# Optimization experiments

Measured on AMD Instinct MI355X. Metric: run time of the kernel, lower is better.

The kernel has to match this reference:

```python
import jax, jax.numpy as jnp
import numpy as np

B, LC, LS, D = 16384, 100, 12, 10  # C:(B,LC,D), x1:(B,LS,D)


def setup_inputs() -> dict:
    key = jax.random.key(0)
    ks = jax.random.split(key, 7)
    u = lambda k, shp: jax.random.uniform(k, shp, jnp.float32, -0.05, 0.05)  # keras 'uniform' init
    return {
        "C": jax.random.normal(ks[0], (B, LC, D), jnp.float32),
        "x1": jax.random.normal(ks[1], (B, LS, D), jnp.float32),
        "W": u(ks[2], (D, D)),      # kernelW (10,10)
        "Ws": u(ks[3], (LS, LS)),   # kernelWs (12,12)
        "Wc": u(ks[4], (LC, LC)),   # kernelWc (100,100)
        "Was": u(ks[5], (D, 1)),    # kernelas (10,1)
        "Wac": u(ks[6], (D, 1)),    # kernelac (10,1)
    }


def reference(C, x1, W, Ws, Wc, Was, Wac):
    # C: (B,100,10), x1: (B,12,10)
    RNN = jnp.swapaxes(x1, 1, 2)                      # (B,10,12)
    f = jnp.einsum('bld,de->ble', C, W)               # (B,100,10)
    F = jnp.tanh(jnp.matmul(f, RNN))                  # (B,100,12)
    s = jnp.einsum('bdl,lm->bdm', RNN, Ws)            # (B,10,12)
    c = jnp.einsum('bdl,lm->bdm', jnp.swapaxes(C, 1, 2), Wc)  # (B,10,100)
    Hs = jnp.tanh(s + jnp.matmul(c, F))               # (B,10,12)
    Hc = jnp.tanh(c + jnp.matmul(s, jnp.swapaxes(F, 1, 2)))   # (B,10,100)
    # softmax over the last (size-1) axis, exactly as K.softmax does here
    As = jax.nn.softmax(jnp.einsum('bdl,do->blo', Hs, Was), axis=-1)  # (B,12,1)
    Ac = jax.nn.softmax(jnp.einsum('bdl,do->blo', Hc, Wac), axis=-1)  # (B,100,1)
    As = jnp.swapaxes(As, 1, 2)                       # (B,1,12)
    Ac = jnp.swapaxes(Ac, 1, 2)                       # (B,1,100)
    sfinal = jnp.matmul(As, jnp.swapaxes(RNN, 1, 2))  # (B,1,10)
    cfinal = jnp.matmul(Ac, C)                        # (B,1,10)
    return jnp.concatenate([sfinal, cfinal], axis=-1) # (B,1,20)
```

## Files before the change

### kernel.cpp

```cpp
#include <hip/hip_runtime.h>
#include <hip/hip_bf16.h>


#define BATCHES 16384

__global__ __launch_bounds__(256) void coattention_sum_kernel(
    const float* __restrict__ C,
    const float* __restrict__ x1,
    float* __restrict__ out)
{
    const int t = threadIdx.x;
    const int lane = t & 63;
    const int q = lane >> 4;
    const int wave = t >> 6;
    const int u = blockIdx.x * 64 + wave * 16 + (lane & 15);
    const int b = u / 5;
    const int p = u - b * 5;

    const float2* __restrict__ cp =
        reinterpret_cast<const float2*>(C) + (size_t)b * 500 + q * 125 + p;
    const float2* __restrict__ xp =
        reinterpret_cast<const float2*>(x1) + (size_t)b * 60 + q * 15 + p;

    float sx = 0.f, sy = 0.f;
#pragma unroll
    for (int l = 0; l < 3; ++l)  { float2 v = xp[l * 5]; sx += v.x; sy += v.y; }

    float cx = 0.f, cy = 0.f;
#pragma unroll
    for (int l = 0; l < 25; ++l) { float2 v = cp[l * 5]; cx += v.x; cy += v.y; }

    sx += __shfl_xor(sx, 16); sy += __shfl_xor(sy, 16);
    cx += __shfl_xor(cx, 16); cy += __shfl_xor(cy, 16);
    sx += __shfl_xor(sx, 32); sy += __shfl_xor(sy, 32);
    cx += __shfl_xor(cx, 32); cy += __shfl_xor(cy, 32);

    if (q == 0) {
        float2* o = reinterpret_cast<float2*>(out) + (size_t)b * 10;
        o[p]     = make_float2(sx, sy);
        o[5 + p] = make_float2(cx, cy);
    }
}

extern "C" void kernel_launch(void* const* d_in, const int* in_sizes, int n_in,
                              void* d_out, int out_size, void* d_ws, size_t ws_size,
                              hipStream_t stream) {
    const float* C  = (const float*)d_in[0];
    const float* x1 = (const float*)d_in[1];
    float* out = (float*)d_out;

    const int units = BATCHES * 5;
    const int grid = units / 64;
    coattention_sum_kernel<<<grid, 256, 0, stream>>>(C, x1, out);
}
```

Before: 17.91 us.

## Stage batch tiles through LDS with coalesced float4 loads before reducing

```diff
diff --git a/kernel.cpp b/kernel.cpp
--- a/kernel.cpp
+++ b/kernel.cpp
@@ -3,40 +3,54 @@
 
 
 #define BATCHES 16384
+#define NB 16
 
-__global__ __launch_bounds__(256) void coattention_sum_kernel(
-    const float* __restrict__ C,
-    const float* __restrict__ x1,
+__global__ __launch_bounds__(320) void coattention_sum_kernel(
+    const float4* __restrict__ C4,
+    const float4* __restrict__ x14,
     float* __restrict__ out)
 {
+    __shared__ __align__(16) float4 lds4[NB * 250 + NB * 30];
+
     const int t = threadIdx.x;
-    const int lane = t & 63;
-    const int q = lane >> 4;
-    const int wave = t >> 6;
-    const int u = blockIdx.x * 64 + wave * 16 + (lane & 15);
-    const int b = u / 5;
-    const int p = u - b * 5;
 
-    const float2* __restrict__ cp =
-        reinterpret_cast<const float2*>(C) + (size_t)b * 500 + q * 125 + p;
-    const float2* __restrict__ xp =
-        reinterpret_cast<const float2*>(x1) + (size_t)b * 60 + q * 15 + p;
+    const float4* __restrict__ Cg = C4 + (size_t)blockIdx.x * (NB * 250);
+    const float4* __restrict__ Xg = x14 + (size_t)blockIdx.x * (NB * 30);
+#pragma unroll
+    for (int k = 0; k < 12; ++k)
+        lds4[k * 320 + t] = Cg[k * 320 + t];
+    if (t < 160)
+        lds4[3840 + t] = Cg[3840 + t];
+    lds4[4000 + t] = Xg[t];
+    if (t < 160)
+        lds4[4320 + t] = Xg[320 + t];
+    __syncthreads();
+
+    const int unit = t >> 2;
+    const int q = t & 3;
+    const int b = unit / 5;
+    const int p = unit - b * 5;
+
+    const float2* __restrict__ lbase = reinterpret_cast<const float2*>(lds4);
+    const float2* __restrict__ lc = lbase + b * 500 + q * 125 + p;
+    const float2* __restrict__ lx = lbase + 8000 + b * 60 + q * 15 + p;
+
+    float cx = 0.f, cy = 0.f;
+#pragma unroll
+    for (int l = 0; l < 25; ++l) { float2 v = lc[l * 5]; cx += v.x; cy += v.y; }
 
     float sx = 0.f, sy = 0.f;
 #pragma unroll
-    for (int l = 0; l < 3; ++l)  { float2 v = xp[l * 5]; sx += v.x; sy += v.y; }
+    for (int l = 0; l < 3; ++l)  { float2 v = lx[l * 5]; sx += v.x; sy += v.y; }
 
-    float cx = 0.f, cy = 0.f;
-#pragma unroll
-    for (int l = 0; l < 25; ++l) { float2 v = cp[l * 5]; cx += v.x; cy += v.y; }
-
-    sx += __shfl_xor(sx, 16); sy += __shfl_xor(sy, 16);
-    cx += __shfl_xor(cx, 16); cy += __shfl_xor(cy, 16);
-    sx += __shfl_xor(sx, 32); sy += __shfl_xor(sy, 32);
-    cx += __shfl_xor(cx, 32); cy += __shfl_xor(cy, 32);
+    cx += __shfl_xor(cx, 1); cy += __shfl_xor(cy, 1);
+    sx += __shfl_xor(sx, 1); sy += __shfl_xor(sy, 1);
+    cx += __shfl_xor(cx, 2); cy += __shfl_xor(cy, 2);
+    sx += __shfl_xor(sx, 2); sy += __shfl_xor(sy, 2);
 
     if (q == 0) {
-        float2* o = reinterpret_cast<float2*>(out) + (size_t)b * 10;
+        float2* o = reinterpret_cast<float2*>(out)
+                  + ((size_t)blockIdx.x * NB + b) * 10;
         o[p]     = make_float2(sx, sy);
         o[5 + p] = make_float2(cx, cy);
     }
@@ -45,11 +59,10 @@
 extern "C" void kernel_launch(void* const* d_in, const int* in_sizes, int n_in,
                               void* d_out, int out_size, void* d_ws, size_t ws_size,
                               hipStream_t stream) {
-    const float* C  = (const float*)d_in[0];
-    const float* x1 = (const float*)d_in[1];
+    const float4* C4  = (const float4*)d_in[0];
+    const float4* x14 = (const float4*)d_in[1];
     float* out = (float*)d_out;
 
-    const int units = BATCHES * 5;
-    const int grid = units / 64;
-    coattention_sum_kernel<<<grid, 256, 0, stream>>>(C, x1, out);
+    const int grid = BATCHES / NB;
+    coattention_sum_kernel<<<grid, 320, 0, stream>>>(C4, x14, out);
 }
```

Measured after the change: 20.85 us. 16.5% more time.
